# Performance work log

Hardware: AMD Instinct MI355X
Metric: run time of the kernel (lower is better)

Reference implementation:

```python
import jax, jax.numpy as jnp
import numpy as np

B, S, HID = 2, 2048, 2048
NH, NKV, D = 32, 4, 64
N_REP = NH // NKV
EPS = 1e-6
ROPE_THETA = 10000.0


def _rotate_half(x):
    h = x.shape[-1] // 2
    return jnp.concatenate([-x[..., h:], x[..., :h]], axis=-1)


def _rmsnorm(x, gamma):
    # RMSNorm over last dim (head_dim)
    return x * jax.lax.rsqrt(jnp.mean(x * x, axis=-1, keepdims=True) + EPS) * gamma


def setup_inputs() -> dict:
    key = jax.random.key(0)
    ks = jax.random.split(key, 8)
    hidden_states = jax.random.normal(ks[0], (B, S, HID), dtype=jnp.float32)
    # rotary cos/sin tables, shape [B, S, D]
    pos = jnp.arange(S, dtype=jnp.float32)
    inv_freq = 1.0 / (ROPE_THETA ** (jnp.arange(0, D, 2, dtype=jnp.float32) / D))
    freqs = pos[:, None] * inv_freq[None, :]            # [S, D/2]
    emb = jnp.concatenate([freqs, freqs], axis=-1)      # [S, D]
    cos = jnp.broadcast_to(jnp.cos(emb)[None], (B, S, D))
    sin = jnp.broadcast_to(jnp.sin(emb)[None], (B, S, D))
    sc = 0.02
    Wq = jax.random.normal(ks[1], (NH * D, HID), dtype=jnp.float32) * sc
    Wk = jax.random.normal(ks[2], (NKV * D, HID), dtype=jnp.float32) * sc
    Wv = jax.random.normal(ks[3], (NKV * D, HID), dtype=jnp.float32) * sc
    Wg = jax.random.normal(ks[4], (NH * D, HID), dtype=jnp.float32) * sc
    Wo = jax.random.normal(ks[5], (HID, NH * D), dtype=jnp.float32) * sc
    q_gamma = jnp.ones((D,), dtype=jnp.float32)
    k_gamma = jnp.ones((D,), dtype=jnp.float32)
    return dict(hidden_states=hidden_states, cos=cos, sin=sin,
                Wq=Wq, Wk=Wk, Wv=Wv, Wg=Wg, Wo=Wo,
                q_gamma=q_gamma, k_gamma=k_gamma)


def reference(hidden_states, cos, sin, Wq, Wk, Wv, Wg, Wo, q_gamma, k_gamma):
    b, s, _ = hidden_states.shape
    q = (hidden_states @ Wq.T).reshape(b, s, NH, D)
    k = (hidden_states @ Wk.T).reshape(b, s, NKV, D)
    v = (hidden_states @ Wv.T).reshape(b, s, NKV, D)
    gate = hidden_states @ Wg.T                       # [B, S, NH*D]
    # per-head RMSNorm on q/k
    q = _rmsnorm(q, q_gamma)
    k = _rmsnorm(k, k_gamma)
    # [B, H, S, D]
    q = q.transpose(0, 2, 1, 3)
    k = k.transpose(0, 2, 1, 3)
    v = v.transpose(0, 2, 1, 3)
    # RoPE (unsqueeze_dim=1)
    c = cos[:, None, :, :]
    sn = sin[:, None, :, :]
    q = q * c + _rotate_half(q) * sn
    k = k * c + _rotate_half(k) * sn
    # GQA: repeat kv heads
    kr = jnp.repeat(k, N_REP, axis=1)
    vr = jnp.repeat(v, N_REP, axis=1)
    scaling = D ** -0.5
    scores = jnp.einsum('bhqd,bhkd->bhqk', q, kr) * scaling
    w = jax.nn.softmax(scores.astype(jnp.float32), axis=-1).astype(q.dtype)
    out = jnp.einsum('bhqk,bhkd->bhqd', w, vr)
    out = out.transpose(0, 2, 1, 3).reshape(b, s, NH * D)
    out = out * jax.nn.sigmoid(gate)
    return out @ Wo.T
```

## Files before the change

kernel.cpp:

```cpp
#include <hip/hip_runtime.h>


#define LOG2E 1.44269504088896340736f

typedef __attribute__((ext_vector_type(4))) float f32x4;
typedef __attribute__((ext_vector_type(8))) short bf16x8;

__device__ __forceinline__ float bf2f(unsigned short u) {
  union { unsigned u; float f; } x; x.u = ((unsigned)u) << 16; return x.f;
}
__device__ __forceinline__ unsigned short f2bf(float f) {
  union { float f; unsigned u; } x; x.f = f;
  unsigned r = x.u + 0x7fffu + ((x.u >> 16) & 1u);
  return (unsigned short)(r >> 16);
}

__device__ __forceinline__ void async16(void* lds, const void* g) {
  __builtin_amdgcn_global_load_lds(
      (const __attribute__((address_space(1))) unsigned*)g,
      (__attribute__((address_space(3))) unsigned*)lds, 16, 0, 0);
}
__device__ __forceinline__ void lds_fence() {
  __asm__ volatile("s_waitcnt lgkmcnt(0)" ::: "memory");
}

__global__ __launch_bounds__(256) void cvt_all(
    const float* __restrict__ s0, const float* __restrict__ s1,
    const float* __restrict__ s2, const float* __restrict__ s3,
    const float* __restrict__ s4, const float* __restrict__ s5,
    unsigned short* __restrict__ d0, unsigned short* __restrict__ d1,
    unsigned short* __restrict__ d2, unsigned short* __restrict__ d3,
    unsigned short* __restrict__ d4, unsigned short* __restrict__ d5) {
  const long total = 5505024;
  const long stride = (long)gridDim.x * 256;
  for (long i = (long)blockIdx.x * 256 + threadIdx.x; i < total; i += stride) {
    const float* s; unsigned short* d; long off;
    if      (i < 2097152) { s = s0; d = d0; off = 0; }
    else if (i < 3145728) { s = s1; d = d1; off = 2097152; }
    else if (i < 3276800) { s = s2; d = d2; off = 3145728; }
    else if (i < 3407872) { s = s3; d = d3; off = 3276800; }
    else if (i < 4456448) { s = s4; d = d4; off = 3407872; }
    else                  { s = s5; d = d5; off = 4456448; }
    long j = i - off;
    float4 v = reinterpret_cast<const float4*>(s)[j];
    ushort4 u;
    u.x = f2bf(v.x); u.y = f2bf(v.y); u.z = f2bf(v.z); u.w = f2bf(v.w);
    reinterpret_cast<ushort4*>(d)[j] = u;
  }
}

__device__ __forceinline__ void gemm_core(
    const unsigned short* __restrict__ A, const unsigned short* __restrict__ W,
    int m0, int n0, unsigned short* lds, f32x4 acc[4][8]) {
  const int tid = threadIdx.x;
  const int w = tid >> 6, l = tid & 63, quad = l >> 4, l16 = l & 15;
  const int wm = (w & 1) * 64, wn = (w >> 1) * 128;
  const int rlo = tid >> 2, ch = tid & 3;

  const f32x4 Z4 = {0.f, 0.f, 0.f, 0.f};
#pragma unroll
  for (int i = 0; i < 4; i++)
#pragma unroll
    for (int j = 0; j < 8; j++) acc[i][j] = Z4;

  const unsigned short* gA =
      A + (size_t)(m0 + rlo) * 2048 + ((ch ^ ((rlo >> 1) & 3)) * 8);
  const unsigned short* gB =
      W + (size_t)(n0 + rlo) * 2048 + ((ch ^ ((rlo >> 1) & 3)) * 8);

  int arow[4], brow[8];
#pragma unroll
  for (int mt = 0; mt < 4; mt++) arow[mt] = (wm + mt * 16 + l16) * 32;
#pragma unroll
  for (int nt = 0; nt < 8; nt++) brow[nt] = (wn + nt * 16 + l16) * 32;
  const int fx = (quad ^ ((l16 >> 1) & 3)) * 8;

  unsigned short* const bA = lds;
  unsigned short* const bB = lds + 12288;

#pragma unroll
  for (int tt = 0; tt < 2; ++tt) {
    const int ko = tt * 32;
    async16(bA + tt * 4096 + tid * 8,        gA + ko);
    async16(bA + tt * 4096 + 2048 + tid * 8, gA + 131072 + ko);
    async16(bB + tt * 8192 + tid * 8,        gB + ko);
    async16(bB + tt * 8192 + 2048 + tid * 8, gB + 131072 + ko);
    async16(bB + tt * 8192 + 4096 + tid * 8, gB + 262144 + ko);
    async16(bB + tt * 8192 + 6144 + tid * 8, gB + 393216 + ko);
  }
  __asm__ volatile("s_waitcnt vmcnt(6)" ::: "memory");
  __builtin_amdgcn_s_barrier();

  int cb = 0;
  for (int t = 0; t < 64; ++t) {
    unsigned short* cA = bA + cb * 4096;
    unsigned short* cB = bB + cb * 8192;

    if (t < 62) {
      int nb = cb + 2; if (nb >= 3) nb -= 3;
      const int ko = (t + 2) * 32;
      async16(bA + nb * 4096 + tid * 8,        gA + ko);
      async16(bA + nb * 4096 + 2048 + tid * 8, gA + 131072 + ko);
      async16(bB + nb * 8192 + tid * 8,        gB + ko);
      async16(bB + nb * 8192 + 2048 + tid * 8, gB + 131072 + ko);
      async16(bB + nb * 8192 + 4096 + tid * 8, gB + 262144 + ko);
      async16(bB + nb * 8192 + 6144 + tid * 8, gB + 393216 + ko);
    }

    bf16x8 af[4], bf[8];
#pragma unroll
    for (int mt = 0; mt < 4; mt++)
      af[mt] = *(const bf16x8*)&cA[arow[mt] + fx];
#pragma unroll
    for (int nt = 0; nt < 8; nt++)
      bf[nt] = *(const bf16x8*)&cB[brow[nt] + fx];

    __builtin_amdgcn_s_setprio(1);
#pragma unroll
    for (int nt = 0; nt < 8; nt++)
#pragma unroll
      for (int mt = 0; mt < 4; mt++)
        acc[mt][nt] = __builtin_amdgcn_mfma_f32_16x16x32_bf16(
            af[mt], bf[nt], acc[mt][nt], 0, 0, 0);
    __builtin_amdgcn_s_setprio(0);

    if (t < 62) {
      __asm__ volatile("s_waitcnt vmcnt(6)" ::: "memory");
    } else if (t == 62) {
      __asm__ volatile("s_waitcnt vmcnt(0)" ::: "memory");
    }
    __builtin_amdgcn_s_barrier();
    cb++; if (cb == 3) cb = 0;
  }
}

__global__ __launch_bounds__(256, 2) void gemm_qkvg(
    const unsigned short* __restrict__ X,
    const unsigned short* __restrict__ Wq, const unsigned short* __restrict__ Wk,
    const unsigned short* __restrict__ Wv, const unsigned short* __restrict__ Wg,
    const float* __restrict__ cosb, const float* __restrict__ sinb,
    const float* __restrict__ qg, const float* __restrict__ kg,
    unsigned short* __restrict__ Qn, unsigned short* __restrict__ Kn,
    unsigned short* __restrict__ Vt, unsigned short* __restrict__ gate) {
  __shared__ __attribute__((aligned(16))) unsigned short lds[36864];
  const int ny = blockIdx.y;
  const unsigned short* W; int n0, type;
  if (ny < 8)       { W = Wq; n0 = ny * 256;        type = 0; }
  else if (ny == 8) { W = Wk; n0 = 0;               type = 1; }
  else if (ny == 9) { W = Wv; n0 = 0;               type = 2; }
  else              { W = Wg; n0 = (ny - 10) * 256; type = 3; }
  const int m0 = blockIdx.x * 128;

  f32x4 acc[4][8];
  gemm_core(X, W, m0, n0, lds, acc);

  const int tid = threadIdx.x;
  const int w = tid >> 6, l = tid & 63, quad = l >> 4, l16 = l & 15;
  const int wm = (w & 1) * 64, wn = (w >> 1) * 128;

  if (type == 3) {
#pragma unroll
    for (int mt = 0; mt < 4; mt++)
#pragma unroll
      for (int r = 0; r < 4; r++) {
        int row = m0 + wm + mt * 16 + quad * 4 + r;
#pragma unroll
        for (int nt = 0; nt < 8; nt++)
          gate[(size_t)row * 2048 + n0 + wn + nt * 16 + l16] =
              f2bf(acc[mt][nt][r]);
      }
    return;
  }
  if (type == 2) {
#pragma unroll
    for (int mt = 0; mt < 4; mt++)
#pragma unroll
      for (int r = 0; r < 4; r++) {
        int row = m0 + wm + mt * 16 + quad * 4 + r;
        int b = row >> 11, s = row & 2047;
#pragma unroll
        for (int nt = 0; nt < 8; nt++) {
          int col = wn + nt * 16 + l16;
          int kvh = col >> 6, d = col & 63;
          Vt[((size_t)(b * 4 + kvh) * 64 + d) * 2048 + s] =
              f2bf(acc[mt][nt][r]);
        }
      }
    return;
  }

  const float* gamma = (type == 0) ? qg : kg;
  const float scale  = (type == 0) ? 0.125f : LOG2E;
  const int hb0 = (n0 + wn) >> 6;
  float gv[8];
#pragma unroll
  for (int nt = 0; nt < 8; nt++) gv[nt] = gamma[(nt & 3) * 16 + l16];

#pragma unroll
  for (int mt = 0; mt < 4; mt++)
#pragma unroll
    for (int r = 0; r < 4; r++) {
      int row = m0 + wm + mt * 16 + quad * 4 + r;
      float ss0 = 0.f, ss1 = 0.f;
#pragma unroll
      for (int nt = 0; nt < 4; nt++) {
        float v = acc[mt][nt][r]; ss0 += v * v;
      }
#pragma unroll
      for (int nt = 4; nt < 8; nt++) {
        float v = acc[mt][nt][r]; ss1 += v * v;
      }
#pragma unroll
      for (int off = 1; off < 16; off <<= 1) {
        ss0 += __shfl_xor(ss0, off);
        ss1 += __shfl_xor(ss1, off);
      }
      float rr0 = rsqrtf(ss0 * (1.0f / 64.0f) + 1e-6f);
      float rr1 = rsqrtf(ss1 * (1.0f / 64.0f) + 1e-6f);
      float xn[8];
#pragma unroll
      for (int nt = 0; nt < 8; nt++)
        xn[nt] = acc[mt][nt][r] * ((nt < 4) ? rr0 : rr1) * gv[nt];
      int b = row >> 11, s = row & 2047;
      unsigned short* dst0 = (type == 0)
          ? Qn + ((size_t)(b * 32 + hb0) * 2048 + s) * 64
          : Kn + ((size_t)(b * 4 + hb0) * 2048 + s) * 64;
      unsigned short* dst1 = (type == 0)
          ? Qn + ((size_t)(b * 32 + hb0 + 1) * 2048 + s) * 64
          : Kn + ((size_t)(b * 4 + hb0 + 1) * 2048 + s) * 64;
#pragma unroll
      for (int nt = 0; nt < 8; nt++) {
        int d = (nt & 3) * 16 + l16;
        float rot = ((nt & 3) < 2) ? -xn[nt ^ 2] : xn[nt ^ 2];
        float cv = cosb[(size_t)row * 64 + d];
        float sv = sinb[(size_t)row * 64 + d];
        float val = (xn[nt] * cv + rot * sv) * scale;
        ((nt < 4) ? dst0 : dst1)[d] = f2bf(val);
      }
    }
}

__global__ __launch_bounds__(256, 2) void gemm_out_k(
    const unsigned short* __restrict__ A, const unsigned short* __restrict__ W,
    float* __restrict__ C) {
  __shared__ __attribute__((aligned(16))) unsigned short lds[36864];
  const int m0 = blockIdx.x * 128, n0 = blockIdx.y * 256;
  f32x4 acc[4][8];
  gemm_core(A, W, m0, n0, lds, acc);
  const int tid = threadIdx.x;
  const int w = tid >> 6, l = tid & 63, quad = l >> 4, l16 = l & 15;
  const int wm = (w & 1) * 64, wn = (w >> 1) * 128;
#pragma unroll
  for (int mt = 0; mt < 4; mt++)
#pragma unroll
    for (int nt = 0; nt < 8; nt++) {
      int row = m0 + wm + mt * 16 + quad * 4;
      int col = n0 + wn + nt * 16 + l16;
#pragma unroll
      for (int r = 0; r < 4; r++)
        C[(size_t)(row + r) * 2048 + col] = acc[mt][nt][r];
    }
}

__global__ __launch_bounds__(256, 4) void attn(
    const unsigned short* __restrict__ Qn, const unsigned short* __restrict__ Kn,
    const unsigned short* __restrict__ Vt, const unsigned short* __restrict__ gate,
    unsigned short* __restrict__ act) {
  __shared__ __attribute__((aligned(16))) unsigned short smem[20480];
  unsigned short* Ps = smem + 16384;

  const int tid = threadIdx.x, w = tid >> 6, l = tid & 63;
  const int quad = l >> 4, l16 = l & 15, l7 = l16 & 7;
  const int bh = blockIdx.y, b = bh >> 5, h = bh & 31, kvh = h >> 3;
  const int q0 = blockIdx.x * 128;

  const unsigned short* Qg = Qn + ((size_t)(b * 32 + h) * 2048 + q0) * 64;
  const unsigned short* Kg = Kn + (size_t)(b * 4 + kvh) * 2048 * 64;
  const unsigned short* Vg = Vt + (size_t)(b * 4 + kvh) * 64 * 2048;
  unsigned short* Pw = Ps + w * 1024;

  const int kq_src = ((tid & 7) ^ ((tid >> 3) & 7)) * 8;

#pragma unroll
  for (int i = 0; i < 4; i++)
    async16(smem + i * 2048 + tid * 8,
            Qg + (size_t)(i * 32 + (tid >> 3)) * 64 + kq_src);
  __syncthreads();
  bf16x8 qf[2][2];
#pragma unroll
  for (int mt = 0; mt < 2; mt++)
#pragma unroll
    for (int ks = 0; ks < 2; ks++) {
      int row = w * 32 + mt * 16 + l16;
      qf[mt][ks] = *(const bf16x8*)&smem[row * 64 + ((ks * 4 + quad) ^ l7) * 8];
    }
  __syncthreads();

  const f32x4 Z4 = {0.f, 0.f, 0.f, 0.f};
  f32x4 O[2][4];
  float lp[2][4];
#pragma unroll
  for (int mt = 0; mt < 2; mt++) {
#pragma unroll
    for (int nt = 0; nt < 4; nt++) O[mt][nt] = Z4;
#pragma unroll
    for (int r = 0; r < 4; r++) lp[mt][r] = 0.f;
  }

#pragma unroll
  for (int i = 0; i < 2; i++) {
    async16(smem + i * 2048 + tid * 8,
            Kg + (size_t)(i * 32 + (tid >> 3)) * 64 + kq_src);
    async16(smem + 4096 + i * 2048 + tid * 8,
            Vg + (size_t)(i * 32 + (tid >> 3)) * 2048 + kq_src);
  }

  for (int kt = 0; kt < 32; kt++) {
    __syncthreads();

    if (kt < 31) {
      unsigned short* nb = smem + ((kt + 1) & 1) * 8192;
      const int s1 = (kt + 1) * 64;
#pragma unroll
      for (int i = 0; i < 2; i++) {
        async16(nb + i * 2048 + tid * 8,
                Kg + (size_t)(s1 + i * 32 + (tid >> 3)) * 64 + kq_src);
        async16(nb + 4096 + i * 2048 + tid * 8,
                Vg + (size_t)(i * 32 + (tid >> 3)) * 2048 + s1 + kq_src);
      }
    }

    unsigned short* Ks  = smem + (kt & 1) * 8192;
    unsigned short* Vts = Ks + 4096;

    f32x4 sc[2][4];
#pragma unroll
    for (int mt = 0; mt < 2; mt++)
#pragma unroll
      for (int nt = 0; nt < 4; nt++) sc[mt][nt] = Z4;
    __builtin_amdgcn_s_setprio(1);
#pragma unroll
    for (int nt = 0; nt < 4; nt++) {
      int row = nt * 16 + l16;
      bf16x8 kf0 = *(const bf16x8*)&Ks[row * 64 + (quad ^ l7) * 8];
      bf16x8 kf1 = *(const bf16x8*)&Ks[row * 64 + ((4 + quad) ^ l7) * 8];
#pragma unroll
      for (int mt = 0; mt < 2; mt++) {
        sc[mt][nt] = __builtin_amdgcn_mfma_f32_16x16x32_bf16(qf[mt][0], kf0, sc[mt][nt], 0, 0, 0);
        sc[mt][nt] = __builtin_amdgcn_mfma_f32_16x16x32_bf16(qf[mt][1], kf1, sc[mt][nt], 0, 0, 0);
      }
    }
    __builtin_amdgcn_s_setprio(0);

#pragma unroll
    for (int ks2 = 0; ks2 < 2; ks2++) {
#pragma unroll
      for (int mt = 0; mt < 2; mt++)
#pragma unroll
        for (int ntl = 0; ntl < 2; ntl++) {
          int nt = ks2 * 2 + ntl;
#pragma unroll
          for (int r = 0; r < 4; r++) {
            float p = __builtin_amdgcn_exp2f(sc[mt][nt][r]);
            union { float f; unsigned u; } x; x.f = p;
            union { unsigned u; float f; } t; t.u = x.u & 0xffff0000u;
            lp[mt][r] += t.f;
            int q = mt * 16 + quad * 4 + r;
            int c = ntl * 2 + (l16 >> 3);
            int phys = c ^ ((q >> 1) & 3);
            Pw[q * 32 + phys * 8 + l7] = (unsigned short)(x.u >> 16);
          }
        }
      lds_fence();

      bf16x8 pf[2];
#pragma unroll
      for (int mt = 0; mt < 2; mt++) {
        int q = mt * 16 + l16;
        int phys = quad ^ ((l16 >> 1) & 3);
        pf[mt] = *(const bf16x8*)&Pw[q * 32 + phys * 8];
      }
      __builtin_amdgcn_s_setprio(1);
#pragma unroll
      for (int nt2 = 0; nt2 < 4; nt2++) {
        int d = nt2 * 16 + l16;
        bf16x8 vf = *(const bf16x8*)&Vts[d * 64 + ((ks2 * 4 + quad) ^ l7) * 8];
#pragma unroll
        for (int mt = 0; mt < 2; mt++)
          O[mt][nt2] = __builtin_amdgcn_mfma_f32_16x16x32_bf16(
              pf[mt], vf, O[mt][nt2], 0, 0, 0);
      }
      __builtin_amdgcn_s_setprio(0);
      lds_fence();
    }
  }

#pragma unroll
  for (int mt = 0; mt < 2; mt++)
#pragma unroll
    for (int r = 0; r < 4; r++) {
      float s = lp[mt][r];
#pragma unroll
      for (int off = 1; off < 16; off <<= 1) s += __shfl_xor(s, off);
      lp[mt][r] = s;
    }

#pragma unroll
  for (int mt = 0; mt < 2; mt++) {
    float inv[4];
#pragma unroll
    for (int r = 0; r < 4; r++) inv[r] = 1.0f / lp[mt][r];
#pragma unroll
    for (int nt = 0; nt < 4; nt++)
#pragma unroll
      for (int r = 0; r < 4; r++) {
        int srow = q0 + w * 32 + mt * 16 + quad * 4 + r;
        int col = h * 64 + nt * 16 + l16;
        size_t off = (size_t)(b * 2048 + srow) * 2048 + col;
        float g = bf2f(gate[off]);
        float sig = 1.0f / (1.0f + __builtin_amdgcn_exp2f(-g * LOG2E));
        act[off] = f2bf(O[mt][nt][r] * inv[r] * sig);
      }
  }
}

extern "C" void kernel_launch(void* const* d_in, const int* in_sizes, int n_in,
                              void* d_out, int out_size, void* d_ws, size_t ws_size,
                              hipStream_t stream) {
  const float* hid  = (const float*)d_in[0];
  const float* cosb = (const float*)d_in[1];
  const float* sinb = (const float*)d_in[2];
  const float* Wq   = (const float*)d_in[3];
  const float* Wk   = (const float*)d_in[4];
  const float* Wv   = (const float*)d_in[5];
  const float* Wg   = (const float*)d_in[6];
  const float* Wo   = (const float*)d_in[7];
  const float* qg   = (const float*)d_in[8];
  const float* kg   = (const float*)d_in[9];
  float* out = (float*)d_out;

  char* ws = (char*)d_ws;
  unsigned short* Xb   = (unsigned short*)(ws);
  unsigned short* WqB  = (unsigned short*)(ws + 16777216);
  unsigned short* WkB  = (unsigned short*)(ws + 25165824);
  unsigned short* WvB  = (unsigned short*)(ws + 26214400);
  unsigned short* WgB  = (unsigned short*)(ws + 27262976);
  unsigned short* WoB  = (unsigned short*)(ws + 35651584);
  unsigned short* gate = (unsigned short*)(ws + 44040192);
  unsigned short* Qn   = (unsigned short*)(ws + 60817408);
  unsigned short* Kn   = (unsigned short*)(ws + 77594624);
  unsigned short* Vt   = (unsigned short*)(ws + 79691776);
  unsigned short* act = WqB;

  cvt_all<<<dim3(2048), dim3(256), 0, stream>>>(
      hid, Wq, Wk, Wv, Wg, Wo, Xb, WqB, WkB, WvB, WgB, WoB);

  gemm_qkvg<<<dim3(32, 18), dim3(256), 0, stream>>>(
      Xb, WqB, WkB, WvB, WgB, cosb, sinb, qg, kg, Qn, Kn, Vt, gate);

  attn<<<dim3(16, 64), dim3(256), 0, stream>>>(Qn, Kn, Vt, gate, act);

  gemm_out_k<<<dim3(32, 8), dim3(256), 0, stream>>>(act, WoB, out);
}
```

Measured before the change: 382.3 us.

## Shrink GEMM tiles to 128x128 with two waves and double buffering

```diff
diff --git a/kernel.cpp b/kernel.cpp
--- a/kernel.cpp
+++ b/kernel.cpp
@@ -54,7 +54,7 @@
     int m0, int n0, unsigned short* lds, f32x4 acc[4][8]) {
   const int tid = threadIdx.x;
   const int w = tid >> 6, l = tid & 63, quad = l >> 4, l16 = l & 15;
-  const int wm = (w & 1) * 64, wn = (w >> 1) * 128;
+  const int wm = w * 64;
   const int rlo = tid >> 2, ch = tid & 3;
 
   const f32x4 Z4 = {0.f, 0.f, 0.f, 0.f};
@@ -72,48 +72,39 @@
 #pragma unroll
   for (int mt = 0; mt < 4; mt++) arow[mt] = (wm + mt * 16 + l16) * 32;
 #pragma unroll
-  for (int nt = 0; nt < 8; nt++) brow[nt] = (wn + nt * 16 + l16) * 32;
+  for (int nt = 0; nt < 8; nt++) brow[nt] = (nt * 16 + l16) * 32;
   const int fx = (quad ^ ((l16 >> 1) & 3)) * 8;
 
-  unsigned short* const bA = lds;
-  unsigned short* const bB = lds + 12288;
-
-#pragma unroll
-  for (int tt = 0; tt < 2; ++tt) {
-    const int ko = tt * 32;
-    async16(bA + tt * 4096 + tid * 8,        gA + ko);
-    async16(bA + tt * 4096 + 2048 + tid * 8, gA + 131072 + ko);
-    async16(bB + tt * 8192 + tid * 8,        gB + ko);
-    async16(bB + tt * 8192 + 2048 + tid * 8, gB + 131072 + ko);
-    async16(bB + tt * 8192 + 4096 + tid * 8, gB + 262144 + ko);
-    async16(bB + tt * 8192 + 6144 + tid * 8, gB + 393216 + ko);
-  }
-  __asm__ volatile("s_waitcnt vmcnt(6)" ::: "memory");
+#pragma unroll
+  for (int p = 0; p < 4; p++) {
+    async16(lds + p * 1024 + tid * 8,        gA + (size_t)p * 32 * 2048);
+    async16(lds + 4096 + p * 1024 + tid * 8, gB + (size_t)p * 32 * 2048);
+  }
+  __asm__ volatile("s_waitcnt vmcnt(0)" ::: "memory");
   __builtin_amdgcn_s_barrier();
 
-  int cb = 0;
   for (int t = 0; t < 64; ++t) {
-    unsigned short* cA = bA + cb * 4096;
-    unsigned short* cB = bB + cb * 8192;
-
-    if (t < 62) {
-      int nb = cb + 2; if (nb >= 3) nb -= 3;
-      const int ko = (t + 2) * 32;
-      async16(bA + nb * 4096 + tid * 8,        gA + ko);
-      async16(bA + nb * 4096 + 2048 + tid * 8, gA + 131072 + ko);
-      async16(bB + nb * 8192 + tid * 8,        gB + ko);
-      async16(bB + nb * 8192 + 2048 + tid * 8, gB + 131072 + ko);
-      async16(bB + nb * 8192 + 4096 + tid * 8, gB + 262144 + ko);
-      async16(bB + nb * 8192 + 6144 + tid * 8, gB + 393216 + ko);
+    unsigned short* cbuf = lds + (t & 1) * 8192;
+
+    if (t < 63) {
+      unsigned short* nbuf = lds + ((t + 1) & 1) * 8192;
+      const int ko = (t + 1) * 32;
+#pragma unroll
+      for (int p = 0; p < 4; p++) {
+        async16(nbuf + p * 1024 + tid * 8,
+                gA + (size_t)p * 32 * 2048 + ko);
+        async16(nbuf + 4096 + p * 1024 + tid * 8,
+                gB + (size_t)p * 32 * 2048 + ko);
+      }
     }
 
     bf16x8 af[4], bf[8];
 #pragma unroll
     for (int mt = 0; mt < 4; mt++)
-      af[mt] = *(const bf16x8*)&cA[arow[mt] + fx];
+      af[mt] = *(const bf16x8*)&cbuf[arow[mt] + fx];
 #pragma unroll
     for (int nt = 0; nt < 8; nt++)
-      bf[nt] = *(const bf16x8*)&cB[brow[nt] + fx];
+      bf[nt] = *(const bf16x8*)&cbuf[4096 + brow[nt] + fx];
 
     __builtin_amdgcn_s_setprio(1);
 #pragma unroll
@@ -124,17 +115,12 @@
             af[mt], bf[nt], acc[mt][nt], 0, 0, 0);
     __builtin_amdgcn_s_setprio(0);
 
-    if (t < 62) {
-      __asm__ volatile("s_waitcnt vmcnt(6)" ::: "memory");
-    } else if (t == 62) {
-      __asm__ volatile("s_waitcnt vmcnt(0)" ::: "memory");
-    }
+    __asm__ volatile("s_waitcnt vmcnt(0)" ::: "memory");
     __builtin_amdgcn_s_barrier();
-    cb++; if (cb == 3) cb = 0;
-  }
-}
-
-__global__ __launch_bounds__(256, 2) void gemm_qkvg(
+  }
+}
+
+__global__ __launch_bounds__(128, 2) void gemm_qkvg(
     const unsigned short* __restrict__ X,
     const unsigned short* __restrict__ Wq, const unsigned short* __restrict__ Wk,
     const unsigned short* __restrict__ Wv, const unsigned short* __restrict__ Wg,
@@ -142,13 +128,13 @@
     const float* __restrict__ qg, const float* __restrict__ kg,
     unsigned short* __restrict__ Qn, unsigned short* __restrict__ Kn,
     unsigned short* __restrict__ Vt, unsigned short* __restrict__ gate) {
-  __shared__ __attribute__((aligned(16))) unsigned short lds[36864];
+  __shared__ __attribute__((aligned(16))) unsigned short lds[16384];
   const int ny = blockIdx.y;
   const unsigned short* W; int n0, type;
-  if (ny < 8)       { W = Wq; n0 = ny * 256;        type = 0; }
-  else if (ny == 8) { W = Wk; n0 = 0;               type = 1; }
-  else if (ny == 9) { W = Wv; n0 = 0;               type = 2; }
-  else              { W = Wg; n0 = (ny - 10) * 256; type = 3; }
+  if (ny < 16)      { W = Wq; n0 = ny * 128;        type = 0; }
+  else if (ny < 18) { W = Wk; n0 = (ny - 16) * 128; type = 1; }
+  else if (ny < 20) { W = Wv; n0 = (ny - 18) * 128; type = 2; }
+  else              { W = Wg; n0 = (ny - 20) * 128; type = 3; }
   const int m0 = blockIdx.x * 128;
 
   f32x4 acc[4][8];
@@ -156,7 +142,7 @@
 
   const int tid = threadIdx.x;
   const int w = tid >> 6, l = tid & 63, quad = l >> 4, l16 = l & 15;
-  const int wm = (w & 1) * 64, wn = (w >> 1) * 128;
+  const int wm = w * 64;
 
   if (type == 3) {
 #pragma unroll
@@ -166,7 +152,7 @@
         int row = m0 + wm + mt * 16 + quad * 4 + r;
 #pragma unroll
         for (int nt = 0; nt < 8; nt++)
-          gate[(size_t)row * 2048 + n0 + wn + nt * 16 + l16] =
+          gate[(size_t)row * 2048 + n0 + nt * 16 + l16] =
               f2bf(acc[mt][nt][r]);
       }
     return;
@@ -180,7 +166,7 @@
         int b = row >> 11, s = row & 2047;
 #pragma unroll
         for (int nt = 0; nt < 8; nt++) {
-          int col = wn + nt * 16 + l16;
+          int col = n0 + nt * 16 + l16;
           int kvh = col >> 6, d = col & 63;
           Vt[((size_t)(b * 4 + kvh) * 64 + d) * 2048 + s] =
               f2bf(acc[mt][nt][r]);
@@ -191,7 +177,7 @@
 
   const float* gamma = (type == 0) ? qg : kg;
   const float scale  = (type == 0) ? 0.125f : LOG2E;
-  const int hb0 = (n0 + wn) >> 6;
+  const int hb0 = n0 >> 6;
   float gv[8];
 #pragma unroll
   for (int nt = 0; nt < 8; nt++) gv[nt] = gamma[(nt & 3) * 16 + l16];
@@ -240,22 +226,22 @@
     }
 }
 
-__global__ __launch_bounds__(256, 2) void gemm_out_k(
+__global__ __launch_bounds__(128, 2) void gemm_out_k(
     const unsigned short* __restrict__ A, const unsigned short* __restrict__ W,
     float* __restrict__ C) {
-  __shared__ __attribute__((aligned(16))) unsigned short lds[36864];
-  const int m0 = blockIdx.x * 128, n0 = blockIdx.y * 256;
+  __shared__ __attribute__((aligned(16))) unsigned short lds[16384];
+  const int m0 = blockIdx.x * 128, n0 = blockIdx.y * 128;
   f32x4 acc[4][8];
   gemm_core(A, W, m0, n0, lds, acc);
   const int tid = threadIdx.x;
   const int w = tid >> 6, l = tid & 63, quad = l >> 4, l16 = l & 15;
-  const int wm = (w & 1) * 64, wn = (w >> 1) * 128;
+  const int wm = w * 64;
 #pragma unroll
   for (int mt = 0; mt < 4; mt++)
 #pragma unroll
     for (int nt = 0; nt < 8; nt++) {
       int row = m0 + wm + mt * 16 + quad * 4;
-      int col = n0 + wn + nt * 16 + l16;
+      int col = n0 + nt * 16 + l16;
 #pragma unroll
       for (int r = 0; r < 4; r++)
         C[(size_t)(row + r) * 2048 + col] = acc[mt][nt][r];
@@ -455,10 +441,10 @@
   cvt_all<<<dim3(2048), dim3(256), 0, stream>>>(
       hid, Wq, Wk, Wv, Wg, Wo, Xb, WqB, WkB, WvB, WgB, WoB);
 
-  gemm_qkvg<<<dim3(32, 18), dim3(256), 0, stream>>>(
+  gemm_qkvg<<<dim3(32, 36), dim3(128), 0, stream>>>(
       Xb, WqB, WkB, WvB, WgB, cosb, sinb, qg, kg, Qn, Kn, Vt, gate);
 
   attn<<<dim3(16, 64), dim3(256), 0, stream>>>(Qn, Kn, Vt, gate, act);
 
-  gemm_out_k<<<dim3(32, 8), dim3(256), 0, stream>>>(act, WoB, out);
-}
+  gemm_out_k<<<dim3(32, 16), dim3(128), 0, stream>>>(act, WoB, out);
+}
```

Measured after the change: 378.2 us. No clear change (-1.1%).
